# Kernel tuning notes

Measured on AMD Instinct MI355X. Metric: run time of the kernel, lower is better.

## Reference

```python
import math
import jax, jax.numpy as jnp
import numpy as np

HIDDEN = 2048
NUM_HEADS = 16
HEAD_DIM = HIDDEN // NUM_HEADS  # 128
KV_RANK = 512
ROPE_DIM = 64
MAX_POS = 131072
ORIG_POS = 8192
BASE = 500000.0
BETA_FAST, BETA_SLOW = 32.0, 1.0
B, S = 2, 2048
EPS = 1e-6


def yarn_inv_freq():
    scaling = MAX_POS / ORIG_POS
    pos_freqs = BASE ** (np.arange(0, ROPE_DIM, 2, dtype=np.float64) / ROPE_DIM)
    extrap = 1.0 / pos_freqs
    interp = 1.0 / (scaling * pos_freqs)
    low = max(math.floor(ROPE_DIM * math.log(ORIG_POS / (BETA_FAST * 2 * math.pi)) / (2 * math.log(BASE))), 0)
    high = min(math.ceil(ROPE_DIM * math.log(ORIG_POS / (BETA_SLOW * 2 * math.pi)) / (2 * math.log(BASE))), ROPE_DIM - 1)
    i = np.arange(ROPE_DIM // 2, dtype=np.float64)
    smooth = np.clip((i - low) / max(high - low, 1), 0.0, 1.0)
    inv_freq = (1.0 - smooth) * interp + smooth * extrap
    return np.asarray(inv_freq, dtype=np.float32)


def yarn_cos_sin(seq_len, dtype):
    inv_freq = jnp.asarray(yarn_inv_freq())  # [rope/2]
    pos = jnp.arange(seq_len, dtype=jnp.float32)
    freqs = pos[:, None] * inv_freq[None, :]          # [S, rope/2]
    emb = jnp.concatenate([freqs, freqs], axis=-1)    # [S, rope]
    scaling = MAX_POS / ORIG_POS
    mscale = (0.1 * math.log(scaling) + 1.0) if scaling > 1 else 1.0
    cos = (jnp.cos(emb) * mscale).astype(dtype)[None]  # [1, S, rope]
    sin = (jnp.sin(emb) * mscale).astype(dtype)[None]
    return cos, sin


def rotate_half(x):
    x1, x2 = jnp.split(x, 2, axis=-1)
    return jnp.concatenate([-x2, x1], axis=-1)


def rms_norm(x, w):
    xf = x.astype(jnp.float32)
    var = jnp.mean(xf * xf, axis=-1, keepdims=True)
    return (w * (xf * jax.lax.rsqrt(var + EPS))).astype(x.dtype)


def setup_inputs() -> dict:
    key = jax.random.key(0)
    ks = jax.random.split(key, 5)
    return {
        'hidden_states': jax.random.normal(ks[0], (B, S, HIDDEN), jnp.float32),
        'q_w': jax.random.normal(ks[1], (NUM_HEADS * HEAD_DIM, HIDDEN), jnp.float32) * 0.02,
        'kv_a_w': jax.random.normal(ks[2], (KV_RANK + ROPE_DIM, HIDDEN), jnp.float32) * 0.02,
        'kv_b_w': jax.random.normal(ks[3], (NUM_HEADS * HEAD_DIM * 2, KV_RANK), jnp.float32) * 0.02,
        'o_w': jax.random.normal(ks[4], (HIDDEN, NUM_HEADS * HEAD_DIM), jnp.float32) * 0.02,
        'kv_norm_w': jnp.ones((KV_RANK,), jnp.float32),
    }


def reference(hidden_states, q_w, kv_a_w, kv_b_w, o_w, kv_norm_w):
    b, s, _ = hidden_states.shape
    # Q projection -> [B, H, S, D]
    q = hidden_states @ q_w.T
    q = q.reshape(b, s, NUM_HEADS, HEAD_DIM).transpose(0, 2, 1, 3)
    # KV compression: split off rope part (unused, matching source) and latent
    kv_compress = hidden_states @ kv_a_w.T               # [B, S, rope + rank]
    kv_latent = kv_compress[..., ROPE_DIM:]              # [B, S, rank]
    kv_latent = rms_norm(kv_latent, kv_norm_w)
    kv = kv_latent @ kv_b_w.T                            # [B, S, H*D*2]
    kv = kv.reshape(b, s, NUM_HEADS, 2, HEAD_DIM)
    k = kv[:, :, :, 0].transpose(0, 2, 1, 3)             # [B, H, S, D]
    v = kv[:, :, :, 1].transpose(0, 2, 1, 3)
    # Partial RoPE on first ROPE_DIM dims
    cos, sin = yarn_cos_sin(s, q.dtype)                  # [1, S, rope]
    cos = cos[:, None]                                   # [1, 1, S, rope]
    sin = sin[:, None]
    q_pe, k_pe = q[..., :ROPE_DIM], k[..., :ROPE_DIM]
    q_pe = q_pe * cos + rotate_half(q_pe) * sin
    k_pe = k_pe * cos + rotate_half(k_pe) * sin
    q = jnp.concatenate([q_pe, q[..., ROPE_DIM:]], axis=-1)
    k = jnp.concatenate([k_pe, k[..., ROPE_DIM:]], axis=-1)
    # SDPA (no mask), softmax in fp32
    scale = HEAD_DIM ** -0.5
    scores = jnp.einsum('bhqd,bhkd->bhqk', q, k) * scale
    attn = jax.nn.softmax(scores.astype(jnp.float32), axis=-1).astype(q.dtype)
    out = jnp.einsum('bhqk,bhkd->bhqd', attn, v)         # [B, H, S, D]
    out = out.transpose(0, 2, 1, 3).reshape(b, s, NUM_HEADS * HEAD_DIM)
    return out @ o_w.T
```

## Files before the change

### kernel.cpp

```cpp
#include <hip/hip_runtime.h>

typedef unsigned short u16;
typedef unsigned int u32;
typedef __attribute__((ext_vector_type(4))) float f32x4;
typedef __attribute__((ext_vector_type(8))) short short8;

#define S_LEN 2048
#define BATCH 2
#define HID 2048
#define NH 16
#define HD 128
#define KVR 512
#define TOKENS 4096
#define QSCALE 0.12751879523243842f

__device__ __forceinline__ u32 f2bf(float f) {
  u32 b = __float_as_uint(f);
  return (b + 0x7FFFu + ((b >> 16) & 1u)) >> 16;
}
__device__ __forceinline__ float bf2f(u16 u) {
  return __uint_as_float(((u32)u) << 16);
}
__device__ __forceinline__ void gl16(const void* g, void* l) {
  __builtin_amdgcn_global_load_lds((const __attribute__((address_space(1))) void*)g,
                                   (__attribute__((address_space(3))) void*)l, 16, 0, 0);
}
__device__ __forceinline__ u32 cvtpk(float a, float b) {
  u32 r;
  asm("v_cvt_pk_bf16_f32 %0, %1, %2" : "=v"(r) : "v"(a), "v"(b));
  return r;
}

__global__ __launch_bounds__(256) void convert_all(
    const float* __restrict__ s0, u16* __restrict__ d0, int n0,
    const float* __restrict__ s1, u16* __restrict__ d1, int n1,
    const float* __restrict__ s2, u16* __restrict__ d2, int n2,
    const float* __restrict__ s3, u16* __restrict__ d3, int n3,
    const float* __restrict__ s4, u16* __restrict__ d4, int n4c) {
  const int stride = gridDim.x * blockDim.x;
  const int total = n0 + n1 + n2 + n3 + n4c;
  for (int i = blockIdx.x * blockDim.x + threadIdx.x; i < total; i += stride) {
    const float* s; u16* d; int j = i;
    if (j < n0) { s = s0; d = d0; }
    else { j -= n0;
      if (j < n1) { s = s1; d = d1; }
      else { j -= n1;
        if (j < n2) { s = s2; d = d2; }
        else { j -= n2;
          if (j < n3) { s = s3; d = d3; }
          else { j -= n3; s = s4; d = d4; }
        }
      }
    }
    float4 v = reinterpret_cast<const float4*>(s)[j];
    uint2 o;
    o.x = f2bf(v.x) | (f2bf(v.y) << 16);
    o.y = f2bf(v.z) | (f2bf(v.w) << 16);
    reinterpret_cast<uint2*>(d)[j] = o;
  }
}

__global__ __launch_bounds__(256) void yarn_table(float2* __restrict__ cs) {
  int idx = blockIdx.x * blockDim.x + threadIdx.x;
  if (idx >= S_LEN * 32) return;
  int pos = idx >> 5, i = idx & 31;
  double pf = pow(500000.0, (double)i / 32.0);
  double sm = ((double)i - 9.0) / 9.0;
  sm = sm < 0.0 ? 0.0 : (sm > 1.0 ? 1.0 : sm);
  double invf = (1.0 - sm) / (16.0 * pf) + sm / pf;
  float f = (float)pos * (float)invf;
  const float mscale = 1.2772588722239781f;
  cs[idx] = make_float2(cosf(f) * mscale, sinf(f) * mscale);
}

__global__ __launch_bounds__(256) void rmsnorm_kernel(const float* __restrict__ X,
                                                      const float* __restrict__ w,
                                                      u16* __restrict__ out) {
  int wid = threadIdx.x >> 6, lane = threadIdx.x & 63;
  int row = blockIdx.x * 4 + wid;
  const float* xr = X + (size_t)row * KVR;
  float4 v0 = reinterpret_cast<const float4*>(xr)[lane * 2];
  float4 v1 = reinterpret_cast<const float4*>(xr)[lane * 2 + 1];
  float ss = v0.x * v0.x + v0.y * v0.y + v0.z * v0.z + v0.w * v0.w +
             v1.x * v1.x + v1.y * v1.y + v1.z * v1.z + v1.w * v1.w;
  #pragma unroll
  for (int m = 1; m < 64; m <<= 1) ss += __shfl_xor(ss, m);
  float sc = rsqrtf(ss * (1.0f / KVR) + 1e-6f);
  const float* wr = w + lane * 8;
  uint4 o;
  o.x = f2bf(v0.x * sc * wr[0]) | (f2bf(v0.y * sc * wr[1]) << 16);
  o.y = f2bf(v0.z * sc * wr[2]) | (f2bf(v0.w * sc * wr[3]) << 16);
  o.z = f2bf(v1.x * sc * wr[4]) | (f2bf(v1.y * sc * wr[5]) << 16);
  o.w = f2bf(v1.z * sc * wr[6]) | (f2bf(v1.w * sc * wr[7]) << 16);
  reinterpret_cast<uint4*>(out)[(size_t)row * 64 + lane] = o;
}

template<int MODE>
__global__ __launch_bounds__(256) void gemm_bt(const u16* __restrict__ A,
                                               const u16* __restrict__ W,
                                               void* __restrict__ C0v,
                                               void* __restrict__ C1v,
                                               const float2* __restrict__ cs,
                                               int M, int N, int K) {
  __shared__ u16 As[2][128 * 32];
  __shared__ u16 Bs[2][128 * 32];
  const int tid = threadIdx.x;
  const int wid = tid >> 6;
  const int lane = tid & 63;
  const int r16 = lane & 15;
  const int kg = lane >> 4;
  const int nwg = gridDim.x * gridDim.y;
  const int bid = blockIdx.y * gridDim.x + blockIdx.x;
  const int swz = (bid & 7) * (nwg >> 3) + (bid >> 3);
  const int bm = (swz / gridDim.x) * 128;
  const int bn = (swz % gridDim.x) * 128;
  const int wm = (wid >> 1) * 64;
  const int wn = (wid & 1) * 64;
  f32x4 acc[4][4] = {};
  const int srow = tid >> 2;
  const int sslot = tid & 3;
  const int ra = srow, rb = 64 + srow;
  const int ca = sslot ^ ((ra >> 1) & 3);
  const int cb = sslot ^ ((rb >> 1) & 3);
  const u16* a0 = A + (size_t)(bm + ra) * K + ca * 8;
  const u16* a1 = A + (size_t)(bm + rb) * K + cb * 8;
  const u16* b0 = W + (size_t)(bn + ra) * K + ca * 8;
  const u16* b1 = W + (size_t)(bn + rb) * K + cb * 8;

  auto stage = [&](int buf, int kt) {
    gl16(a0 + kt, &As[buf][wid * 512]);
    gl16(a1 + kt, &As[buf][wid * 512 + 2048]);
    gl16(b0 + kt, &Bs[buf][wid * 512]);
    gl16(b1 + kt, &Bs[buf][wid * 512 + 2048]);
  };

  const int NK = K / 32;
  stage(0, 0);
  for (int t = 0; t < NK; ++t) {
    const int cur = t & 1;
    if (t + 1 < NK) {
      stage(cur ^ 1, (t + 1) * 32);
      asm volatile("s_waitcnt vmcnt(4)" ::: "memory");
    } else {
      asm volatile("s_waitcnt vmcnt(0)" ::: "memory");
    }
    __builtin_amdgcn_s_barrier();
    short8 af[4], bfv[4];
    #pragma unroll
    for (int mi = 0; mi < 4; ++mi) {
      int row = wm + mi * 16 + r16;
      af[mi] = *reinterpret_cast<const short8*>(
          &As[cur][row * 32 + ((kg ^ ((row >> 1) & 3)) << 3)]);
    }
    #pragma unroll
    for (int ni = 0; ni < 4; ++ni) {
      int row = wn + ni * 16 + r16;
      bfv[ni] = *reinterpret_cast<const short8*>(
          &Bs[cur][row * 32 + ((kg ^ ((row >> 1) & 3)) << 3)]);
    }
    #pragma unroll
    for (int mi = 0; mi < 4; ++mi)
      #pragma unroll
      for (int ni = 0; ni < 4; ++ni)
        acc[mi][ni] = __builtin_amdgcn_mfma_f32_16x16x32_bf16(af[mi], bfv[ni], acc[mi][ni], 0, 0, 0);
    __builtin_amdgcn_s_barrier();
  }

  if (MODE == 2 || MODE == 3) {
    const bool doRope = (wn == 0) && (MODE == 2 ? (bn < 2048) : ((bn & 128) == 0));
    if (doRope) {
      #pragma unroll
      for (int mi = 0; mi < 4; ++mi) {
        const int t0 = bm + wm + mi * 16 + kg * 4;
        #pragma unroll
        for (int r = 0; r < 4; ++r) {
          const int pos = (t0 + r) & (S_LEN - 1);
          #pragma unroll
          for (int np = 0; np < 2; ++np) {
            float2 c = cs[pos * 32 + np * 16 + r16];
            float x1 = acc[mi][np][r], x2 = acc[mi][np + 2][r];
            acc[mi][np][r] = x1 * c.x - x2 * c.y;
            acc[mi][np + 2][r] = x2 * c.x + x1 * c.y;
          }
        }
      }
    }
  }

  if (MODE == 1) {
    float* C = (float*)C0v;
    #pragma unroll
    for (int mi = 0; mi < 4; ++mi)
      #pragma unroll
      for (int ni = 0; ni < 4; ++ni) {
        size_t base = (size_t)(bm + wm + mi * 16 + kg * 4) * N + (bn + wn + ni * 16 + r16);
        #pragma unroll
        for (int r = 0; r < 4; ++r) C[base + (size_t)r * N] = acc[mi][ni][r];
      }
  } else if (MODE == 2) {
    if (bn < 2048) {
      u16* C = (u16*)C0v;
      #pragma unroll
      for (int mi = 0; mi < 4; ++mi)
        #pragma unroll
        for (int ni = 0; ni < 4; ++ni) {
          size_t base = (size_t)(bm + wm + mi * 16 + kg * 4) * HID + (bn + wn + ni * 16 + r16);
          #pragma unroll
          for (int r = 0; r < 4; ++r) C[base + (size_t)r * HID] = (u16)f2bf(acc[mi][ni][r] * QSCALE);
        }
    } else {
      float* C = (float*)C1v;
      #pragma unroll
      for (int mi = 0; mi < 4; ++mi)
        #pragma unroll
        for (int ni = 0; ni < 4; ++ni) {
          size_t base = (size_t)(bm + wm + mi * 16 + kg * 4) * KVR +
                        (bn - 2048 + wn + ni * 16 + r16);
          #pragma unroll
          for (int r = 0; r < 4; ++r) C[base + (size_t)r * KVR] = acc[mi][ni][r];
        }
    }
  } else if (MODE == 3) {
    if ((bn & 128) == 0) {
      u16* C = (u16*)C0v;
      #pragma unroll
      for (int mi = 0; mi < 4; ++mi)
        #pragma unroll
        for (int ni = 0; ni < 4; ++ni) {
          size_t base = (size_t)(bm + wm + mi * 16 + kg * 4) * N + (bn + wn + ni * 16 + r16);
          #pragma unroll
          for (int r = 0; r < 4; ++r) C[base + (size_t)r * N] = (u16)f2bf(acc[mi][ni][r]);
        }
    } else {
      u16* Vt = (u16*)C1v;
      const int hh = bn >> 8;
      #pragma unroll
      for (int mi = 0; mi < 4; ++mi) {
        const int tok0 = bm + wm + mi * 16 + kg * 4;
        const int bb = tok0 >> 11, s = tok0 & (S_LEN - 1);
        #pragma unroll
        for (int ni = 0; ni < 4; ++ni) {
          const int d = wn + ni * 16 + r16;
          uint2 pk;
          pk.x = cvtpk(acc[mi][ni][0], acc[mi][ni][1]);
          pk.y = cvtpk(acc[mi][ni][2], acc[mi][ni][3]);
          *reinterpret_cast<uint2*>(
              &Vt[((size_t)((bb * 16 + hh) * 128 + d)) * S_LEN + s]) = pk;
        }
      }
    }
  } else {
    u16* C = (u16*)C0v;
    #pragma unroll
    for (int mi = 0; mi < 4; ++mi)
      #pragma unroll
      for (int ni = 0; ni < 4; ++ni) {
        size_t base = (size_t)(bm + wm + mi * 16 + kg * 4) * N + (bn + wn + ni * 16 + r16);
        #pragma unroll
        for (int r = 0; r < 4; ++r) C[base + (size_t)r * N] = (u16)f2bf(acc[mi][ni][r]);
      }
  }
}

#define KVB 64
__global__ __launch_bounds__(256) __attribute__((amdgpu_num_vgpr(128)))
void attn_kernel(const u16* __restrict__ Q,
                 const u16* __restrict__ KV,
                 const u16* __restrict__ Vt,
                 u16* __restrict__ O) {
  __shared__ u16 Ks[2][KVB * 128];
  __shared__ u16 Vs[2][128 * KVB];
  __shared__ u16 Ps[4][2][16 * 64];
  const int tid = threadIdx.x, wid = tid >> 6, lane = tid & 63;
  const int r16 = lane & 15, kg = lane >> 4;
  const int bh = blockIdx.x, b = bh >> 4, h = bh & 15;
  const int q0 = blockIdx.y * 128 + wid * 32;

  short8 qf0[4], qf1[4];
  {
    const size_t qr0 = ((size_t)(b * S_LEN) + q0 + r16) * HID + h * HD;
    #pragma unroll
    for (int ds = 0; ds < 4; ++ds) {
      qf0[ds] = *reinterpret_cast<const short8*>(&Q[qr0 + ds * 32 + kg * 8]);
      qf1[ds] = *reinterpret_cast<const short8*>(&Q[qr0 + (size_t)16 * HID + ds * 32 + kg * 8]);
    }
  }
  asm volatile("s_waitcnt vmcnt(0)" ::: "memory");

  f32x4 oacc0[8] = {}, oacc1[8] = {};
  float m0 = -3.0e38f, l0 = 0.0f, m1 = -3.0e38f, l1 = 0.0f;

  const int krow = wid * 4 + (lane >> 4);
  const int kslot = (lane & 15) ^ (krow & 7);
  const u16* gK = KV + (size_t)(b * S_LEN) * 4096 + h * 256 + (size_t)krow * 4096 + kslot * 8;
  const int vrow = wid * 8 + (lane >> 3);
  const int vslot = (lane & 7) ^ (vrow & 7);
  const u16* gV = Vt + ((size_t)bh * 128 + vrow) * S_LEN + vslot * 8;

  auto stage = [&](int buf, int it) {
    const int k0 = it * KVB;
    #pragma unroll
    for (int c = 0; c < 4; ++c) {
      gl16(gK + (size_t)(k0 + c * 16) * 4096, &Ks[buf][(c * 256 + wid * 64) * 8]);
      gl16(gV + (size_t)c * 32 * S_LEN + k0, &Vs[buf][(c * 256 + wid * 64) * 8]);
    }
  };

  auto qk = [&](const u16* Kc, short8 (&qf)[4], f32x4 (&sc)[4]) {
    #pragma unroll
    for (int nt = 0; nt < 4; ++nt) {
      sc[nt] = (f32x4){0.f, 0.f, 0.f, 0.f};
      const int key = nt * 16 + r16;
      #pragma unroll
      for (int ds = 0; ds < 4; ++ds) {
        short8 kf = *reinterpret_cast<const short8*>(
            &Kc[key * 128 + (((ds * 4 + kg) ^ (r16 & 7)) << 3)]);
        sc[nt] = __builtin_amdgcn_mfma_f32_16x16x32_bf16(kf, qf[ds], sc[nt], 0, 0, 0);
      }
    }
  };

  auto softmax_store = [&](f32x4 (&sc)[4], float& mreg, float& lreg, f32x4 (&oa)[8],
                           u16* psbase) {
    float mx = fmaxf(fmaxf(fmaxf(sc[0][0], sc[0][1]), fmaxf(sc[0][2], sc[0][3])),
                     fmaxf(fmaxf(sc[1][0], sc[1][1]), fmaxf(sc[1][2], sc[1][3])));
    mx = fmaxf(mx, fmaxf(fmaxf(fmaxf(sc[2][0], sc[2][1]), fmaxf(sc[2][2], sc[2][3])),
                         fmaxf(fmaxf(sc[3][0], sc[3][1]), fmaxf(sc[3][2], sc[3][3]))));
    mx = fmaxf(mx, __shfl_xor(mx, 16));
    mx = fmaxf(mx, __shfl_xor(mx, 32));
    if (!__all(mx - mreg <= 8.0f)) {
      float nm = fmaxf(mreg, mx);
      float al = __builtin_amdgcn_exp2f(mreg - nm);
      mreg = nm;
      lreg *= al;
      float ar0 = __shfl(al, kg * 4 + 0), ar1 = __shfl(al, kg * 4 + 1);
      float ar2 = __shfl(al, kg * 4 + 2), ar3 = __shfl(al, kg * 4 + 3);
      #pragma unroll
      for (int db = 0; db < 8; ++db) {
        oa[db][0] *= ar0; oa[db][1] *= ar1; oa[db][2] *= ar2; oa[db][3] *= ar3;
      }
    }
    const float nm = mreg;
    float s0 = 0.f;
    #pragma unroll
    for (int nt = 0; nt < 4; ++nt) {
      float p0 = __builtin_amdgcn_exp2f(sc[nt][0] - nm);
      float p1 = __builtin_amdgcn_exp2f(sc[nt][1] - nm);
      float p2 = __builtin_amdgcn_exp2f(sc[nt][2] - nm);
      float p3 = __builtin_amdgcn_exp2f(sc[nt][3] - nm);
      s0 += (p0 + p1) + (p2 + p3);
      uint2 pk;
      pk.x = cvtpk(p0, p1);
      pk.y = cvtpk(p2, p3);
      *reinterpret_cast<uint2*>(
          &psbase[(r16 * 64 + nt * 16 + kg * 4) ^ ((r16 & 7) << 3)]) = pk;
    }
    s0 += __shfl_xor(s0, 16);
    s0 += __shfl_xor(s0, 32);
    lreg += s0;
  };

  stage(0, 0);
  for (int it = 0; it < S_LEN / KVB; ++it) {
    const int cur = it & 1;
    if (it + 1 < S_LEN / KVB) {
      stage(cur ^ 1, it + 1);
      asm volatile("s_waitcnt vmcnt(8)" ::: "memory");
    } else {
      asm volatile("s_waitcnt vmcnt(0)" ::: "memory");
    }
    __builtin_amdgcn_s_barrier();

    const u16* Kc = &Ks[cur][0];
    f32x4 sc[4];
    qk(Kc, qf0, sc);
    softmax_store(sc, m0, l0, oacc0, &Ps[wid][0][0]);
    __builtin_amdgcn_sched_barrier(0);
    qk(Kc, qf1, sc);
    softmax_store(sc, m1, l1, oacc1, &Ps[wid][1][0]);
    __builtin_amdgcn_sched_barrier(0);

    const u16* Vc = &Vs[cur][0];
    #pragma unroll
    for (int ks = 0; ks < 2; ++ks) {
      const int pidx = (r16 * 64 + ks * 32 + kg * 8) ^ ((r16 & 7) << 3);
      short8 pa0 = *reinterpret_cast<const short8*>(&Ps[wid][0][pidx]);
      short8 pa1 = *reinterpret_cast<const short8*>(&Ps[wid][1][pidx]);
      #pragma unroll
      for (int db = 0; db < 8; ++db) {
        const int drow = db * 16 + r16;
        short8 vf = *reinterpret_cast<const short8*>(
            &Vc[drow * 64 + (((ks * 4 + kg) ^ (r16 & 7)) << 3)]);
        oacc0[db] = __builtin_amdgcn_mfma_f32_16x16x32_bf16(pa0, vf, oacc0[db], 0, 0, 0);
        oacc1[db] = __builtin_amdgcn_mfma_f32_16x16x32_bf16(pa1, vf, oacc1[db], 0, 0, 0);
      }
    }
    __builtin_amdgcn_s_barrier();
  }

  {
    float li0 = 1.0f / l0, li1 = 1.0f / l1;
    float lr0[4], lr1[4];
    #pragma unroll
    for (int r = 0; r < 4; ++r) {
      lr0[r] = __shfl(li0, kg * 4 + r);
      lr1[r] = __shfl(li1, kg * 4 + r);
    }
    #pragma unroll
    for (int db = 0; db < 8; ++db)
      #pragma unroll
      for (int r = 0; r < 4; ++r) {
        size_t i0 = ((size_t)(b * S_LEN) + q0 + kg * 4 + r) * HID + h * HD + db * 16 + r16;
        O[i0] = (u16)f2bf(oacc0[db][r] * lr0[r]);
        O[i0 + (size_t)16 * HID] = (u16)f2bf(oacc1[db][r] * lr1[r]);
      }
  }
}

extern "C" void kernel_launch(void* const* d_in, const int* in_sizes, int n_in,
                              void* d_out, int out_size, void* d_ws, size_t ws_size,
                              hipStream_t stream) {
  (void)in_sizes; (void)n_in; (void)out_size; (void)ws_size;
  const float* hidden = (const float*)d_in[0];
  const float* q_w    = (const float*)d_in[1];
  const float* kv_a_w = (const float*)d_in[2];
  const float* kv_b_w = (const float*)d_in[3];
  const float* o_w    = (const float*)d_in[4];
  const float* nw     = (const float*)d_in[5];

  char* ws = (char*)d_ws;
  size_t off = 0;
  auto carve = [&](size_t n) { void* p = ws + off; off += (n + 255) & ~(size_t)255; return p; };
  u16* h_bf    = (u16*)carve((size_t)TOKENS * HID * 2);
  u16* qaw_bf  = (u16*)carve((size_t)2560 * HID * 2);
  u16* kvbw_bf = (u16*)carve((size_t)4096 * KVR * 2);
  u16* ow_bf   = (u16*)carve((size_t)HID * HID * 2);
  u16* q_bf    = (u16*)carve((size_t)TOKENS * HID * 2);
  float* lat_f = (float*)carve((size_t)TOKENS * KVR * 4);
  u16* lat_bf  = (u16*)carve((size_t)TOKENS * KVR * 2);
  u16* kv_bf   = (u16*)carve((size_t)TOKENS * 4096 * 2);
  float2* cs_t = (float2*)carve((size_t)S_LEN * 32 * 8);
  u16* attn_bf = (u16*)carve((size_t)TOKENS * HID * 2);
  u16* vt_bf   = h_bf;

  dim3 blk(256);

  convert_all<<<dim3(2048), blk, 0, stream>>>(
      hidden, h_bf, TOKENS * HID / 4,
      q_w, qaw_bf, HID * HID / 4,
      kv_a_w + 64 * HID, qaw_bf + (size_t)2048 * HID, KVR * HID / 4,
      kv_b_w, kvbw_bf, 4096 * KVR / 4,
      o_w, ow_bf, HID * HID / 4);
  yarn_table<<<dim3(S_LEN * 32 / 256), blk, 0, stream>>>(cs_t);

  gemm_bt<2><<<dim3(2560 / 128, TOKENS / 128), blk, 0, stream>>>(
      h_bf, qaw_bf, q_bf, lat_f, cs_t, TOKENS, 2560, HID);
  rmsnorm_kernel<<<dim3(TOKENS / 4), blk, 0, stream>>>(lat_f, nw, lat_bf);
  gemm_bt<3><<<dim3(4096 / 128, TOKENS / 128), blk, 0, stream>>>(
      lat_bf, kvbw_bf, kv_bf, vt_bf, cs_t, TOKENS, 4096, KVR);

  attn_kernel<<<dim3(BATCH * NH, S_LEN / 128), blk, 0, stream>>>(q_bf, kv_bf, vt_bf, attn_bf);

  gemm_bt<1><<<dim3(HID / 128, TOKENS / 128), blk, 0, stream>>>(
      attn_bf, ow_bf, (float*)d_out, nullptr, cs_t, TOKENS, HID, HID);
}
```

Measured before the change: 244.6 us.

## Split attention over two KV halves and merge partial outputs in a combine kernel

The attention grid gains a z dimension of 2, so each block handles half of the key sequence. Each block writes its unnormalized partial output plus its running max and sum, and a new combine kernel merges the two halves with log-sum-exp weights. Shared memory drops to a single K/V buffer and interleaved QK/PV per 16-row half, which roughly halves LDS per block so more blocks can sit on a CU. In exchange, the explicit double-buffered prefetch is gone, and there is an extra kernel plus extra global traffic for the partial results. Split 0's partials are stored in the unused V half of the KV buffer.

```diff
diff --git a/kernel.cpp b/kernel.cpp
--- a/kernel.cpp
+++ b/kernel.cpp
@@ -267,14 +267,17 @@
 void attn_kernel(const u16* __restrict__ Q,
                  const u16* __restrict__ KV,
                  const u16* __restrict__ Vt,
-                 u16* __restrict__ O) {
-  __shared__ u16 Ks[2][KVB * 128];
-  __shared__ u16 Vs[2][128 * KVB];
-  __shared__ u16 Ps[4][2][16 * 64];
+                 u16* __restrict__ P0,
+                 u16* __restrict__ P1,
+                 float2* __restrict__ lse) {
+  __shared__ u16 Ks[KVB * 128];
+  __shared__ u16 Vs[128 * KVB];
+  __shared__ u16 Ps[4][16 * 64];
   const int tid = threadIdx.x, wid = tid >> 6, lane = tid & 63;
   const int r16 = lane & 15, kg = lane >> 4;
   const int bh = blockIdx.x, b = bh >> 4, h = bh & 15;
   const int q0 = blockIdx.y * 128 + wid * 32;
+  const int split = blockIdx.z;
 
   short8 qf0[4], qf1[4];
   {
@@ -285,7 +288,6 @@
       qf1[ds] = *reinterpret_cast<const short8*>(&Q[qr0 + (size_t)16 * HID + ds * 32 + kg * 8]);
     }
   }
-  asm volatile("s_waitcnt vmcnt(0)" ::: "memory");
 
   f32x4 oacc0[8] = {}, oacc1[8] = {};
   float m0 = -3.0e38f, l0 = 0.0f, m1 = -3.0e38f, l1 = 0.0f;
@@ -297,16 +299,15 @@
   const int vslot = (lane & 7) ^ (vrow & 7);
   const u16* gV = Vt + ((size_t)bh * 128 + vrow) * S_LEN + vslot * 8;
 
-  auto stage = [&](int buf, int it) {
-    const int k0 = it * KVB;
+  auto stage = [&](int k0) {
     #pragma unroll
     for (int c = 0; c < 4; ++c) {
-      gl16(gK + (size_t)(k0 + c * 16) * 4096, &Ks[buf][(c * 256 + wid * 64) * 8]);
-      gl16(gV + (size_t)c * 32 * S_LEN + k0, &Vs[buf][(c * 256 + wid * 64) * 8]);
+      gl16(gK + (size_t)(k0 + c * 16) * 4096, &Ks[(c * 256 + wid * 64) * 8]);
+      gl16(gV + (size_t)c * 32 * S_LEN + k0, &Vs[(c * 256 + wid * 64) * 8]);
     }
   };
 
-  auto qk = [&](const u16* Kc, short8 (&qf)[4], f32x4 (&sc)[4]) {
+  auto qk = [&](short8 (&qf)[4], f32x4 (&sc)[4]) {
     #pragma unroll
     for (int nt = 0; nt < 4; ++nt) {
       sc[nt] = (f32x4){0.f, 0.f, 0.f, 0.f};
@@ -314,14 +315,13 @@
       #pragma unroll
       for (int ds = 0; ds < 4; ++ds) {
         short8 kf = *reinterpret_cast<const short8*>(
-            &Kc[key * 128 + (((ds * 4 + kg) ^ (r16 & 7)) << 3)]);
+            &Ks[key * 128 + (((ds * 4 + kg) ^ (r16 & 7)) << 3)]);
         sc[nt] = __builtin_amdgcn_mfma_f32_16x16x32_bf16(kf, qf[ds], sc[nt], 0, 0, 0);
       }
     }
   };
 
-  auto softmax_store = [&](f32x4 (&sc)[4], float& mreg, float& lreg, f32x4 (&oa)[8],
-                           u16* psbase) {
+  auto softmax_store = [&](f32x4 (&sc)[4], float& mreg, float& lreg, f32x4 (&oa)[8]) {
     float mx = fmaxf(fmaxf(fmaxf(sc[0][0], sc[0][1]), fmaxf(sc[0][2], sc[0][3])),
                      fmaxf(fmaxf(sc[1][0], sc[1][1]), fmaxf(sc[1][2], sc[1][3])));
     mx = fmaxf(mx, fmaxf(fmaxf(fmaxf(sc[2][0], sc[2][1]), fmaxf(sc[2][2], sc[2][3])),
@@ -353,68 +353,91 @@
       pk.x = cvtpk(p0, p1);
       pk.y = cvtpk(p2, p3);
       *reinterpret_cast<uint2*>(
-          &psbase[(r16 * 64 + nt * 16 + kg * 4) ^ ((r16 & 7) << 3)]) = pk;
+          &Ps[wid][(r16 * 64 + nt * 16 + kg * 4) ^ ((r16 & 7) << 3)]) = pk;
     }
     s0 += __shfl_xor(s0, 16);
     s0 += __shfl_xor(s0, 32);
     lreg += s0;
   };
 
-  stage(0, 0);
-  for (int it = 0; it < S_LEN / KVB; ++it) {
-    const int cur = it & 1;
-    if (it + 1 < S_LEN / KVB) {
-      stage(cur ^ 1, it + 1);
-      asm volatile("s_waitcnt vmcnt(8)" ::: "memory");
-    } else {
-      asm volatile("s_waitcnt vmcnt(0)" ::: "memory");
-    }
-    __builtin_amdgcn_s_barrier();
-
-    const u16* Kc = &Ks[cur][0];
-    f32x4 sc[4];
-    qk(Kc, qf0, sc);
-    softmax_store(sc, m0, l0, oacc0, &Ps[wid][0][0]);
-    __builtin_amdgcn_sched_barrier(0);
-    qk(Kc, qf1, sc);
-    softmax_store(sc, m1, l1, oacc1, &Ps[wid][1][0]);
-    __builtin_amdgcn_sched_barrier(0);
-
-    const u16* Vc = &Vs[cur][0];
+  auto pv = [&](f32x4 (&oa)[8]) {
     #pragma unroll
     for (int ks = 0; ks < 2; ++ks) {
       const int pidx = (r16 * 64 + ks * 32 + kg * 8) ^ ((r16 & 7) << 3);
-      short8 pa0 = *reinterpret_cast<const short8*>(&Ps[wid][0][pidx]);
-      short8 pa1 = *reinterpret_cast<const short8*>(&Ps[wid][1][pidx]);
+      short8 pa = *reinterpret_cast<const short8*>(&Ps[wid][pidx]);
       #pragma unroll
       for (int db = 0; db < 8; ++db) {
         const int drow = db * 16 + r16;
         short8 vf = *reinterpret_cast<const short8*>(
-            &Vc[drow * 64 + (((ks * 4 + kg) ^ (r16 & 7)) << 3)]);
-        oacc0[db] = __builtin_amdgcn_mfma_f32_16x16x32_bf16(pa0, vf, oacc0[db], 0, 0, 0);
-        oacc1[db] = __builtin_amdgcn_mfma_f32_16x16x32_bf16(pa1, vf, oacc1[db], 0, 0, 0);
-      }
-    }
-    __builtin_amdgcn_s_barrier();
+            &Vs[drow * 64 + (((ks * 4 + kg) ^ (r16 & 7)) << 3)]);
+        oa[db] = __builtin_amdgcn_mfma_f32_16x16x32_bf16(pa, vf, oa[db], 0, 0, 0);
+      }
+    }
+  };
+
+  const int kbase = split * (S_LEN / 2);
+  for (int it = 0; it < (S_LEN / 2) / KVB; ++it) {
+    stage(kbase + it * KVB);
+    __syncthreads();
+
+    f32x4 sc[4];
+    qk(qf0, sc);
+    softmax_store(sc, m0, l0, oacc0);
+    pv(oacc0);
+    __builtin_amdgcn_sched_barrier(0);
+    qk(qf1, sc);
+    softmax_store(sc, m1, l1, oacc1);
+    pv(oacc1);
+    __syncthreads();
   }
 
   {
-    float li0 = 1.0f / l0, li1 = 1.0f / l1;
-    float lr0[4], lr1[4];
-    #pragma unroll
-    for (int r = 0; r < 4; ++r) {
-      lr0[r] = __shfl(li0, kg * 4 + r);
-      lr1[r] = __shfl(li1, kg * 4 + r);
-    }
+    u16* Op;
+    size_t stride;
+    if (split == 0) { Op = P0 + h * 256 + 128; stride = 4096; }
+    else            { Op = P1 + h * 128;       stride = 2048; }
     #pragma unroll
     for (int db = 0; db < 8; ++db)
       #pragma unroll
       for (int r = 0; r < 4; ++r) {
-        size_t i0 = ((size_t)(b * S_LEN) + q0 + kg * 4 + r) * HID + h * HD + db * 16 + r16;
-        O[i0] = (u16)f2bf(oacc0[db][r] * lr0[r]);
-        O[i0 + (size_t)16 * HID] = (u16)f2bf(oacc1[db][r] * lr1[r]);
-      }
-  }
+        size_t row = (size_t)(b * S_LEN) + q0 + kg * 4 + r;
+        Op[row * stride + db * 16 + r16] = (u16)f2bf(oacc0[db][r]);
+        Op[(row + 16) * stride + db * 16 + r16] = (u16)f2bf(oacc1[db][r]);
+      }
+    if (kg == 0) {
+      float2* L = lse + (size_t)split * (32 * S_LEN) + (size_t)bh * S_LEN;
+      L[q0 + r16] = make_float2(m0, l0);
+      L[q0 + 16 + r16] = make_float2(m1, l1);
+    }
+  }
+}
+
+__global__ __launch_bounds__(256) void combine_kernel(const u16* __restrict__ P0,
+                                                      u16* __restrict__ P1,
+                                                      const float2* __restrict__ lse) {
+  const int row = blockIdx.x * 16 + (threadIdx.x >> 4);
+  const int tok = row >> 4, h = row & 15;
+  const int b = tok >> 11, q = tok & (S_LEN - 1);
+  const int bh = b * 16 + h;
+  float2 a0 = lse[(size_t)bh * S_LEN + q];
+  float2 a1 = lse[(size_t)32 * S_LEN + (size_t)bh * S_LEN + q];
+  float M = fmaxf(a0.x, a1.x);
+  float e0 = __builtin_amdgcn_exp2f(a0.x - M);
+  float e1 = __builtin_amdgcn_exp2f(a1.x - M);
+  float dn = 1.0f / (a0.y * e0 + a1.y * e1);
+  float w0 = e0 * dn, w1 = e1 * dn;
+  const int dg = (threadIdx.x & 15) * 8;
+  const u16* p0 = P0 + (size_t)tok * 4096 + h * 256 + 128 + dg;
+  u16* p1 = P1 + (size_t)tok * 2048 + h * 128 + dg;
+  uint4 v0 = *reinterpret_cast<const uint4*>(p0);
+  uint4 v1 = *reinterpret_cast<const uint4*>(p1);
+  const u16* s0 = reinterpret_cast<const u16*>(&v0);
+  const u16* s1 = reinterpret_cast<const u16*>(&v1);
+  u16 o[8] __attribute__((aligned(16)));
+  #pragma unroll
+  for (int j = 0; j < 8; ++j)
+    o[j] = (u16)f2bf(bf2f(s0[j]) * w0 + bf2f(s1[j]) * w1);
+  *reinterpret_cast<uint4*>(p1) = *reinterpret_cast<const uint4*>(o);
 }
 
 extern "C" void kernel_launch(void* const* d_in, const int* in_sizes, int n_in,
@@ -442,6 +465,7 @@
   float2* cs_t = (float2*)carve((size_t)S_LEN * 32 * 8);
   u16* attn_bf = (u16*)carve((size_t)TOKENS * HID * 2);
   u16* vt_bf   = h_bf;
+  float2* lse  = (float2*)lat_f;
 
   dim3 blk(256);
 
@@ -459,7 +483,9 @@
   gemm_bt<3><<<dim3(4096 / 128, TOKENS / 128), blk, 0, stream>>>(
       lat_bf, kvbw_bf, kv_bf, vt_bf, cs_t, TOKENS, 4096, KVR);
 
-  attn_kernel<<<dim3(BATCH * NH, S_LEN / 128), blk, 0, stream>>>(q_bf, kv_bf, vt_bf, attn_bf);
+  attn_kernel<<<dim3(BATCH * NH, S_LEN / 128, 2), blk, 0, stream>>>(
+      q_bf, kv_bf, vt_bf, kv_bf, attn_bf, lse);
+  combine_kernel<<<dim3(TOKENS * NH / 16), blk, 0, stream>>>(kv_bf, attn_bf, lse);
 
   gemm_bt<1><<<dim3(HID / 128, TOKENS / 128), blk, 0, stream>>>(
       attn_bf, ow_bf, (float*)d_out, nullptr, cs_t, TOKENS, HID, HID);
```

After: 268.4 us. +9.7%, slower.
